# Kernel optimization log

Measured on AMD Instinct MI355X. Metric: run time of the kernel, lower is better.

The kernel has to match this reference:

```python
import jax, jax.numpy as jnp
import numpy as np

B, N, F, T, O, E = 4, 30000, 32, 12, 64, 480000


def setup_inputs() -> dict:
    key = jax.random.key(0)
    ks = jax.random.split(key, 20)
    s = 0.05
    inp = {
        "X": jax.random.normal(ks[0], (B, N, F, T), dtype=jnp.float32),
        "edge_index": jax.random.randint(ks[1], (2, E), 0, N, dtype=jnp.int64),
        # GCNConv weights for the three gates (num_layers=1 -> single conv each)
        "Wg_z": jax.random.normal(ks[2], (F, O), dtype=jnp.float32) * s,
        "bg_z": jnp.zeros((O,), jnp.float32),
        "Wg_r": jax.random.normal(ks[3], (F, O), dtype=jnp.float32) * s,
        "bg_r": jnp.zeros((O,), jnp.float32),
        "Wg_h": jax.random.normal(ks[4], (F, O), dtype=jnp.float32) * s,
        "bg_h": jnp.zeros((O,), jnp.float32),
        # gate Linear(2*O, O) weights
        "Wl_z": jax.random.normal(ks[5], (2 * O, O), dtype=jnp.float32) * s,
        "bl_z": jnp.zeros((O,), jnp.float32),
        "Wl_r": jax.random.normal(ks[6], (2 * O, O), dtype=jnp.float32) * s,
        "bl_r": jnp.zeros((O,), jnp.float32),
        "Wl_h": jax.random.normal(ks[7], (2 * O, O), dtype=jnp.float32) * s,
        "bl_h": jnp.zeros((O,), jnp.float32),
        # A3TGCN per-period attention and final readout Linear(O, T)
        "att": jax.random.normal(ks[8], (T,), dtype=jnp.float32),
        "W_out": jax.random.normal(ks[9], (O, T), dtype=jnp.float32) * s,
        "b_out": jnp.zeros((T,), jnp.float32),
    }
    return inp


def reference(X, edge_index, Wg_z, bg_z, Wg_r, bg_r, Wg_h, bg_h,
              Wl_z, bl_z, Wl_r, bl_r, Wl_h, bl_h, att, W_out, b_out):
    src, dst = edge_index[0], edge_index[1]
    n = X.shape[1]
    # GCN symmetric normalization with self-loops: deg = in-degree + 1
    deg = jnp.zeros((n,), X.dtype).at[dst].add(1.0) + 1.0
    dis = jax.lax.rsqrt(deg)  # deg^{-1/2}
    edge_norm = (dis[src] * dis[dst])[None, :, None]  # [1,E,1]
    self_norm = (dis * dis)[None, :, None]            # [1,N,1]

    def gcn_conv(x, W, b):  # x: [B,N,F] -> [B,N,O]
        xw = jnp.einsum('bnf,fo->bno', x, W)
        agg = jnp.zeros_like(xw).at[:, dst, :].add(xw[:, src, :] * edge_norm)
        return agg + xw * self_norm + b

    H0 = jnp.zeros((X.shape[0], n, Wg_z.shape[1]), X.dtype)  # H defaults to zeros
    probs = jax.nn.softmax(att)

    def step(acc, inp):
        x_t, p = inp  # x_t: [B,N,F]
        Z = jax.nn.sigmoid(jnp.concatenate([gcn_conv(x_t, Wg_z, bg_z), H0], -1) @ Wl_z + bl_z)
        R = jax.nn.sigmoid(jnp.concatenate([gcn_conv(x_t, Wg_r, bg_r), H0], -1) @ Wl_r + bl_r)
        Ht = jnp.tanh(jnp.concatenate([gcn_conv(x_t, Wg_h, bg_h), H0 * R], -1) @ Wl_h + bl_h)
        Hn = Z * H0 + (1.0 - Z) * Ht
        return acc + p * Hn, None

    Xt = jnp.moveaxis(X, -1, 0)  # [T,B,N,F]
    H_acc, _ = jax.lax.scan(step, jnp.zeros_like(H0), (Xt, probs))
    # TemporalGNN head: ReLU + Linear(O, periods)
    return jax.nn.relu(H_acc) @ W_out + b_out  # [B,N,T]
```

## Files before the change

kernel.cpp:

```cpp
#include <hip/hip_runtime.h>
#include <hip/hip_bf16.h>
#include <hip/hip_fp16.h>


#define FDIM 32
#define TDIM 12
#define ODIM 64
#define BDIM 4

typedef _Float16 half8v __attribute__((ext_vector_type(8)));
typedef float float4v __attribute__((ext_vector_type(4)));

__global__ __launch_bounds__(256) void kA(
    const float4* __restrict__ Xin, uint2* __restrict__ Xh, int n4, int cvtB,
    const int* __restrict__ dstE, int* __restrict__ counts, int E, int cntB,
    const float* __restrict__ Wg_z, const float* __restrict__ bg_z,
    const float* __restrict__ Wl_z, const float* __restrict__ bl_z,
    const float* __restrict__ Wg_h, const float* __restrict__ bg_h,
    const float* __restrict__ Wl_h, const float* __restrict__ bl_h,
    const float* __restrict__ att,
    float* __restrict__ Wz, float* __restrict__ bz,
    float* __restrict__ Wh, float* __restrict__ bh,
    float* __restrict__ probs) {
    const int bid = blockIdx.x;
    const int tid = threadIdx.x;
    if (bid < cvtB) {
        int i = bid * 256 + tid;
        const int stride = cvtB * 256;
        for (; i < n4; i += stride) {
            const float4 v = Xin[i];
            __half2 h0 = __floats2half2_rn(v.x, v.y);
            __half2 h1 = __floats2half2_rn(v.z, v.w);
            uint2 u;
            u.x = *reinterpret_cast<unsigned*>(&h0);
            u.y = *reinterpret_cast<unsigned*>(&h1);
            Xh[i] = u;
        }
    } else if (bid < cvtB + cntB) {
        int e = (bid - cvtB) * 256 + tid;
        if (e < E) atomicAdd(&counts[dstE[e]], 1);
    } else {
        for (int i = tid; i < FDIM * ODIM; i += 256) {
            int f = i >> 6, o = i & 63;
            float az = 0.f, ah = 0.f;
            for (int k = 0; k < ODIM; k++) {
                az += Wg_z[f * ODIM + k] * Wl_z[k * ODIM + o];
                ah += Wg_h[f * ODIM + k] * Wl_h[k * ODIM + o];
            }
            Wz[i] = az;
            Wh[i] = ah;
        }
        if (tid < ODIM) {
            float az = bl_z[tid], ah = bl_h[tid];
            for (int k = 0; k < ODIM; k++) {
                az += bg_z[k] * Wl_z[k * ODIM + tid];
                ah += bg_h[k] * Wl_h[k * ODIM + tid];
            }
            bz[tid] = az;
            bh[tid] = ah;
        }
        if (tid == 0) {
            float m = -1e30f;
            for (int t = 0; t < TDIM; t++) m = fmaxf(m, att[t]);
            float e[TDIM], s = 0.f;
            for (int t = 0; t < TDIM; t++) { e[t] = expf(att[t] - m); s += e[t]; }
            for (int t = 0; t < TDIM; t++) probs[t] = e[t] / s;
        }
    }
}

__global__ __launch_bounds__(1024) void k_scan(const int* __restrict__ counts,
                                               int* __restrict__ offsets,
                                               float* __restrict__ dis,
                                               int* __restrict__ fill,
                                               int2* __restrict__ csr, int N) {
    __shared__ int wsum[16];
    __shared__ int sCarry;
    const int tid = threadIdx.x;
    const int lane = tid & 63;
    const int wv = tid >> 6;
    if (tid == 0) sCarry = 0;
    __syncthreads();
    for (int base = 0; base < N; base += 1024) {
        int i = base + tid;
        int v = (i < N) ? (counts[i] + 1) : 0;
        int s = v;
        for (int off = 1; off < 64; off <<= 1) {
            int t = __shfl_up(s, off, 64);
            if (lane >= off) s += t;
        }
        if (lane == 63) wsum[wv] = s;
        __syncthreads();
        if (wv == 0 && lane < 16) {
            int ws = wsum[lane];
            for (int off = 1; off < 16; off <<= 1) {
                int t = __shfl_up(ws, off, 64);
                if (lane >= off) ws += t;
            }
            wsum[lane] = ws;
        }
        __syncthreads();
        int carry = sCarry;
        int wpre = (wv > 0) ? wsum[wv - 1] : 0;
        if (i < N) {
            const int off0 = carry + wpre + s - v;
            offsets[i] = off0;
            const float d = 1.0f / sqrtf((float)v);
            dis[i] = d;
            fill[i] = 1;
            const float nm = d * d;
            __half2 mh = __floats2half2_rn(nm, nm);
            csr[off0] = make_int2(i, *(int*)&mh);
        }
        __syncthreads();
        if (tid == 0) sCarry = carry + wsum[15];
        __syncthreads();
    }
    if (tid == 0) offsets[N] = sCarry;
}

__global__ void k_scatter(const int* __restrict__ src, const int* __restrict__ dst,
                          const int* __restrict__ offsets, int* __restrict__ fill,
                          const float* __restrict__ dis,
                          int2* __restrict__ csr, int E) {
    int e = blockIdx.x * 256 + threadIdx.x;
    if (e < E) {
        int s = src[e], d = dst[e];
        int pos = offsets[d] + atomicAdd(&fill[d], 1);
        float nm = dis[s] * dis[d];
        __half2 mh = __floats2half2_rn(nm, nm);
        csr[pos] = make_int2(s, *(int*)&mh);
    }
}

__device__ __forceinline__ float sigm(float x) { return 1.f / (1.f + __expf(-x)); }
__device__ __forceinline__ float tanhfast(float x) { return 1.f - 2.f / (1.f + __expf(2.f * x)); }

#define HPACC(mhI, v, hs0, hs1, hs2, hs3)                                      \
    {                                                                          \
        int mi_ = (mhI);                                                       \
        __half2 mh_ = *(__half2*)&mi_;                                         \
        hs0 = __hfma2(mh_, *(__half2*)&(v).x, hs0);                            \
        hs1 = __hfma2(mh_, *(__half2*)&(v).y, hs1);                            \
        hs2 = __hfma2(mh_, *(__half2*)&(v).z, hs2);                            \
        hs3 = __hfma2(mh_, *(__half2*)&(v).w, hs3);                            \
    }

#define HFLUSH(hs0, hs1, hs2, hs3)                                             \
    {                                                                          \
        float2 t_;                                                             \
        t_ = __half22float2(hs0); a0 += t_.x; a1 += t_.y;                      \
        t_ = __half22float2(hs1); a2 += t_.x; a3 += t_.y;                      \
        t_ = __half22float2(hs2); a4 += t_.x; a5 += t_.y;                      \
        t_ = __half22float2(hs3); a6 += t_.x; a7 += t_.y;                      \
        hs0 = hzero; hs1 = hzero; hs2 = hzero; hs3 = hzero;                    \
    }

#define LOADB(dst, Wsrc, jt)                                                   \
    {                                                                          \
        _Pragma("unroll") for (int r_ = 0; r_ < 8; r_++)                       \
            dst[r_] = (_Float16)Wsrc[(kg * 8 + r_) * ODIM + (jt) * 16 + c];    \
    }

#define EPI(qv, dzv, dhv, bzv, bhv)                                            \
    {                                                                          \
        float s_ = 0.f;                                                        \
        {  const float zf_ = dzv[0] + bzv, hf_ = dhv[0] + bhv;                 \
           const float u_ = __expf(-zf_), v_ = __expf(2.f * hf_);              \
           s_ += pr0 * u_ * (v_ - 1.f) *                                       \
                 __builtin_amdgcn_rcpf((1.f + u_) * (1.f + v_)); }             \
        {  const float zf_ = dzv[1] + bzv, hf_ = dhv[1] + bhv;                 \
           const float u_ = __expf(-zf_), v_ = __expf(2.f * hf_);              \
           s_ += pr1 * u_ * (v_ - 1.f) *                                       \
                 __builtin_amdgcn_rcpf((1.f + u_) * (1.f + v_)); }             \
        {  const float zf_ = dzv[2] + bzv, hf_ = dhv[2] + bhv;                 \
           const float u_ = __expf(-zf_), v_ = __expf(2.f * hf_);              \
           s_ += pr2 * u_ * (v_ - 1.f) *                                       \
                 __builtin_amdgcn_rcpf((1.f + u_) * (1.f + v_)); }             \
        {  const float zf_ = dzv[3] + bzv, hf_ = dhv[3] + bhv;                 \
           const float u_ = __expf(-zf_), v_ = __expf(2.f * hf_);              \
           s_ += pr3 * u_ * (v_ - 1.f) *                                       \
                 __builtin_amdgcn_rcpf((1.f + u_) * (1.f + v_)); }             \
        s_ += __shfl_xor(s_, 16, 64);                                          \
        s_ += __shfl_xor(s_, 32, 64);                                          \
        qv = s_;                                                               \
    }

__global__ __launch_bounds__(256, 4) void k_main_w(
    const uint4* __restrict__ Xh, const int* __restrict__ offs,
    const int2* __restrict__ csr,
    const float* __restrict__ Wz, const float* __restrict__ bz,
    const float* __restrict__ Wh, const float* __restrict__ bh,
    const float* __restrict__ probs, const float* __restrict__ Wout,
    const float* __restrict__ bout, float* __restrict__ out, int N) {
    __shared__ float sY[4][16 * 36 + 4];

    const int tid = threadIdx.x;
    const int wv = tid >> 6;
    const int lane = tid & 63;
    const int lanec = lane < 47 ? lane : 47;
    const int c = lane & 15;
    const int kg = lane >> 4;

    half8v wzf0, wzf1, wzf2, wzf3, whf0, whf1, whf2, whf3;
    LOADB(wzf0, Wz, 0) LOADB(wzf1, Wz, 1) LOADB(wzf2, Wz, 2) LOADB(wzf3, Wz, 3)
    LOADB(whf0, Wh, 0) LOADB(whf1, Wh, 1) LOADB(whf2, Wh, 2) LOADB(whf3, Wh, 3)
    half8v wo0, wo1;
#pragma unroll
    for (int r_ = 0; r_ < 8; r_++) {
        wo0[r_] = (_Float16)((c < TDIM) ? Wout[(kg * 8 + r_) * TDIM + c] : 0.f);
        wo1[r_] = (_Float16)((c < TDIM) ? Wout[(32 + kg * 8 + r_) * TDIM + c] : 0.f);
    }
    const float bz0 = bz[c], bz1 = bz[16 + c], bz2 = bz[32 + c], bz3 = bz[48 + c];
    const float bh0 = bh[c], bh1 = bh[16 + c], bh2 = bh[32 + c], bh3 = bh[48 + c];
    const float pr0 = (kg * 4 + 0 < TDIM) ? probs[kg * 4 + 0] : 0.f;
    const float pr1 = (kg * 4 + 1 < TDIM) ? probs[kg * 4 + 1] : 0.f;
    const float pr2 = (kg * 4 + 2 < TDIM) ? probs[kg * 4 + 2] : 0.f;
    const float pr3 = (kg * 4 + 3 < TDIM) ? probs[kg * 4 + 3] : 0.f;
    const float bo = (lane < TDIM) ? bout[lane] : 0.f;
    const __half2 hzero = __float2half2_rn(0.f);

    float* __restrict__ sy = sY[wv];
    const int strideT = gridDim.x * 4;
    const int totalTasks = N * BDIM;

    int task0 = blockIdx.x * 4 + wv;
    if (task0 >= totalTasks) return;
    int b = task0 / N;
    int n = task0 - b * N;

    while (true) {
        const int bs = __builtin_amdgcn_readfirstlane(b);
        const int ns = __builtin_amdgcn_readfirstlane(n);
        const unsigned rowB = (unsigned)bs * (unsigned)N;
        const int begS = __builtin_amdgcn_readfirstlane(offs[ns]);
        const int endS = __builtin_amdgcn_readfirstlane(offs[ns + 1]);

        float a0 = 0.f, a1 = 0.f, a2 = 0.f, a3 = 0.f,
              a4 = 0.f, a5 = 0.f, a6 = 0.f, a7 = 0.f;
        __half2 hA0 = hzero, hA1 = hzero, hA2 = hzero, hA3 = hzero;
        __half2 hB0 = hzero, hB1 = hzero, hB2 = hzero, hB3 = hzero;
        int j = begS;
        for (; j + 8 <= endS; j += 8) {
            const int2 e0 = csr[j + 0], e1 = csr[j + 1], e2 = csr[j + 2], e3 = csr[j + 3];
            const int2 e4 = csr[j + 4], e5 = csr[j + 5], e6 = csr[j + 6], e7 = csr[j + 7];
            const uint4 x0 = Xh[(rowB + (unsigned)e0.x) * 48u + lanec];
            const uint4 x1 = Xh[(rowB + (unsigned)e1.x) * 48u + lanec];
            const uint4 x2 = Xh[(rowB + (unsigned)e2.x) * 48u + lanec];
            const uint4 x3 = Xh[(rowB + (unsigned)e3.x) * 48u + lanec];
            const uint4 x4 = Xh[(rowB + (unsigned)e4.x) * 48u + lanec];
            const uint4 x5 = Xh[(rowB + (unsigned)e5.x) * 48u + lanec];
            const uint4 x6 = Xh[(rowB + (unsigned)e6.x) * 48u + lanec];
            const uint4 x7 = Xh[(rowB + (unsigned)e7.x) * 48u + lanec];
            HPACC(e0.y, x0, hA0, hA1, hA2, hA3);
            HPACC(e1.y, x1, hA0, hA1, hA2, hA3);
            HPACC(e2.y, x2, hA0, hA1, hA2, hA3);
            HPACC(e3.y, x3, hA0, hA1, hA2, hA3);
            HPACC(e4.y, x4, hB0, hB1, hB2, hB3);
            HPACC(e5.y, x5, hB0, hB1, hB2, hB3);
            HPACC(e6.y, x6, hB0, hB1, hB2, hB3);
            HPACC(e7.y, x7, hB0, hB1, hB2, hB3);
            HFLUSH(hA0, hA1, hA2, hA3);
            HFLUSH(hB0, hB1, hB2, hB3);
        }
        for (; j < endS; ++j) {
            const int2 e = csr[j];
            const uint4 xv = Xh[(rowB + (unsigned)e.x) * 48u + lanec];
            HPACC(e.y, xv, hA0, hA1, hA2, hA3);
        }
        HFLUSH(hA0, hA1, hA2, hA3);

        if (lane < 48) {
            int flat = lane * 8;
            int f = flat / 12;
            int t = flat - f * 12;
#pragma unroll
            for (int k = 0; k < 8; k++) {
                float av = (k == 0) ? a0 : (k == 1) ? a1 : (k == 2) ? a2 :
                           (k == 3) ? a3 : (k == 4) ? a4 : (k == 5) ? a5 :
                           (k == 6) ? a6 : a7;
                sy[t * 36 + f] = av;
                t++;
                if (t == TDIM) { t = 0; f++; }
            }
        }

        half8v af;
        if (c < TDIM) {
            const float4* yp = (const float4*)&sy[c * 36 + kg * 8];
            const float4 y0 = yp[0];
            const float4 y1 = yp[1];
            af[0] = (_Float16)y0.x; af[1] = (_Float16)y0.y;
            af[2] = (_Float16)y0.z; af[3] = (_Float16)y0.w;
            af[4] = (_Float16)y1.x; af[5] = (_Float16)y1.y;
            af[6] = (_Float16)y1.z; af[7] = (_Float16)y1.w;
        } else {
            af[0] = (_Float16)0.f; af[1] = (_Float16)0.f;
            af[2] = (_Float16)0.f; af[3] = (_Float16)0.f;
            af[4] = (_Float16)0.f; af[5] = (_Float16)0.f;
            af[6] = (_Float16)0.f; af[7] = (_Float16)0.f;
        }

        const float4v zero4 = {0.f, 0.f, 0.f, 0.f};
        float4v dz0 = __builtin_amdgcn_mfma_f32_16x16x32_f16(af, wzf0, zero4, 0, 0, 0);
        float4v dz1 = __builtin_amdgcn_mfma_f32_16x16x32_f16(af, wzf1, zero4, 0, 0, 0);
        float4v dz2 = __builtin_amdgcn_mfma_f32_16x16x32_f16(af, wzf2, zero4, 0, 0, 0);
        float4v dz3 = __builtin_amdgcn_mfma_f32_16x16x32_f16(af, wzf3, zero4, 0, 0, 0);
        float4v dh0 = __builtin_amdgcn_mfma_f32_16x16x32_f16(af, whf0, zero4, 0, 0, 0);
        float4v dh1 = __builtin_amdgcn_mfma_f32_16x16x32_f16(af, whf1, zero4, 0, 0, 0);
        float4v dh2 = __builtin_amdgcn_mfma_f32_16x16x32_f16(af, whf2, zero4, 0, 0, 0);
        float4v dh3 = __builtin_amdgcn_mfma_f32_16x16x32_f16(af, whf3, zero4, 0, 0, 0);

        float q0, q1, q2, q3;
        EPI(q0, dz0, dh0, bz0, bh0)
        EPI(q1, dz1, dh1, bz1, bh1)
        EPI(q2, dz2, dh2, bz2, bh2)
        EPI(q3, dz3, dh3, bz3, bh3)
        const float accOwn = (kg == 0) ? q0 : (kg == 1) ? q1 : (kg == 2) ? q2 : q3;

        const float r = fmaxf(accOwn, 0.f);
        half8v ra0, ra1;
#pragma unroll
        for (int j2 = 0; j2 < 8; j2++) {
            ra0[j2] = (_Float16)__shfl(r, (kg << 3) + j2, 64);
            ra1[j2] = (_Float16)__shfl(r, 32 + (kg << 3) + j2, 64);
        }
        float4v dro = __builtin_amdgcn_mfma_f32_16x16x32_f16(ra0, wo0, zero4, 0, 0, 0);
        dro = __builtin_amdgcn_mfma_f32_16x16x32_f16(ra1, wo1, dro, 0, 0, 0);
        if (lane < TDIM)
            out[(rowB + (unsigned)n) * TDIM + lane] = dro[0] + bo;

        n += strideT;
        if (n >= N) { n -= N; b++; }
        if (b >= BDIM) break;
    }
}

__global__ __launch_bounds__(384) void k_main_f(
    const float* __restrict__ X, const int* __restrict__ offsets,
    const int2* __restrict__ csr, const float* __restrict__ dis,
    const float* __restrict__ Wz, const float* __restrict__ bz,
    const float* __restrict__ Wh, const float* __restrict__ bh,
    const float* __restrict__ probs, const float* __restrict__ Wout,
    const float* __restrict__ bout, float* __restrict__ out, int N) {
    const int tid = threadIdx.x;
    const int lane = tid & 63;

    __shared__ float4 sY4[BDIM][96];
    __shared__ float sAcc[BDIM][ODIM];
    __shared__ float sWout[ODIM * TDIM];
    __shared__ float sBout[TDIM];

    for (int i = tid; i < ODIM * TDIM; i += 384) sWout[i] = Wout[i];
    if (tid < TDIM) sBout[tid] = bout[tid];

    const int o = tid & 63;
    const int w = tid >> 6;
    float wzr[FDIM], whr[FDIM];
#pragma unroll
    for (int f = 0; f < FDIM; f++) {
        wzr[f] = Wz[f * ODIM + o];
        whr[f] = Wh[f * ODIM + o];
    }
    const float bzo = bz[o], bho = bh[o];
    const int t0 = w, t1 = w + 6;
    const float p0 = probs[t0], p1 = probs[t1];

    const int b = tid / 96;
    const int q = tid - b * 96;
    const float4* __restrict__ Xq = (const float4*)X;
    const unsigned rowBase = (unsigned)b * (unsigned)N;

    for (int n = blockIdx.x; n < N; n += gridDim.x) {
        if (tid < BDIM * ODIM) ((float*)sAcc)[tid] = 0.f;

        const int beg = offsets[n], end = offsets[n + 1];
        float4 A0 = make_float4(0.f, 0.f, 0.f, 0.f);
        float4 A1 = A0, A2 = A0, A3 = A0;

        for (int ebase = beg; ebase < end; ebase += 64) {
            const int cnt2 = min(64, end - ebase);
            int esrc = 0;
            float enm = 0.f;
            if (ebase + lane < end) {
                const int2 e = csr[ebase + lane];
                esrc = e.x;
                int ey = e.y;
                enm = __half22float2(*(__half2*)&ey).x;
            }
            int j = 0;
            for (; j + 4 <= cnt2; j += 4) {
                const int s0 = __shfl(esrc, j + 0, 64), s1 = __shfl(esrc, j + 1, 64);
                const int s2 = __shfl(esrc, j + 2, 64), s3 = __shfl(esrc, j + 3, 64);
                const float m0 = __shfl(enm, j + 0, 64), m1 = __shfl(enm, j + 1, 64);
                const float m2 = __shfl(enm, j + 2, 64), m3 = __shfl(enm, j + 3, 64);
                const float4 u0 = Xq[(rowBase + s0) * 96u + q];
                const float4 u1 = Xq[(rowBase + s1) * 96u + q];
                const float4 u2 = Xq[(rowBase + s2) * 96u + q];
                const float4 u3 = Xq[(rowBase + s3) * 96u + q];
                A0.x += m0 * u0.x; A0.y += m0 * u0.y; A0.z += m0 * u0.z; A0.w += m0 * u0.w;
                A1.x += m1 * u1.x; A1.y += m1 * u1.y; A1.z += m1 * u1.z; A1.w += m1 * u1.w;
                A2.x += m2 * u2.x; A2.y += m2 * u2.y; A2.z += m2 * u2.z; A2.w += m2 * u2.w;
                A3.x += m3 * u3.x; A3.y += m3 * u3.y; A3.z += m3 * u3.z; A3.w += m3 * u3.w;
            }
            for (; j < cnt2; j++) {
                const int s = __shfl(esrc, j, 64);
                const float m = __shfl(enm, j, 64);
                const float4 u = Xq[(rowBase + s) * 96u + q];
                A0.x += m * u.x; A0.y += m * u.y; A0.z += m * u.z; A0.w += m * u.w;
            }
        }
        A0.x += (A1.x + A2.x) + A3.x;
        A0.y += (A1.y + A2.y) + A3.y;
        A0.z += (A1.z + A2.z) + A3.z;
        A0.w += (A1.w + A2.w) + A3.w;
        sY4[b][q] = A0;
        __syncthreads();

#pragma unroll
        for (int bb = 0; bb < BDIM; bb++) {
            const float* yb = (const float*)sY4[bb];
            float z0 = bzo, z1 = bzo, h0 = bho, h1 = bho;
#pragma unroll
            for (int f = 0; f < FDIM; f++) {
                float ya = yb[f * TDIM + t0];
                float yc = yb[f * TDIM + t1];
                z0 += ya * wzr[f]; h0 += ya * whr[f];
                z1 += yc * wzr[f]; h1 += yc * whr[f];
            }
            float contrib = p0 * (1.f - sigm(z0)) * tanhfast(h0)
                          + p1 * (1.f - sigm(z1)) * tanhfast(h1);
            atomicAdd(&sAcc[bb][o], contrib);
        }
        __syncthreads();

        if (tid < BDIM * TDIM) {
            int ob = tid / TDIM, jj = tid - ob * TDIM;
            float v = sBout[jj];
#pragma unroll
            for (int o2 = 0; o2 < ODIM; o2++) {
                v += fmaxf(sAcc[ob][o2], 0.f) * sWout[o2 * TDIM + jj];
            }
            out[(unsigned)(ob * N + n) * TDIM + jj] = v;
        }
        __syncthreads();
    }
}

extern "C" void kernel_launch(void* const* d_in, const int* in_sizes, int n_in,
                              void* d_out, int out_size, void* d_ws, size_t ws_size,
                              hipStream_t stream) {
    const float* X    = (const float*)d_in[0];
    const int*   ei   = (const int*)d_in[1];
    const float* Wg_z = (const float*)d_in[2];
    const float* bg_z = (const float*)d_in[3];
    const float* Wg_h = (const float*)d_in[6];
    const float* bg_h = (const float*)d_in[7];
    const float* Wl_z = (const float*)d_in[8];
    const float* bl_z = (const float*)d_in[9];
    const float* Wl_h = (const float*)d_in[12];
    const float* bl_h = (const float*)d_in[13];
    const float* att  = (const float*)d_in[14];
    const float* Wout = (const float*)d_in[15];
    const float* bout = (const float*)d_in[16];
    float* out = (float*)d_out;

    const int E = in_sizes[1] / 2;
    const int N = in_sizes[0] / (BDIM * FDIM * TDIM);
    const size_t xElems = (size_t)BDIM * N * FDIM * TDIM;
    const size_t xhBytes = xElems * 2;
    const size_t csrBytes = (size_t)(E + N) * 8;
    const size_t restBytes = (size_t)N * 4 * 4 + 64 + csrBytes + 20000;
    const bool useH = ws_size >= xhBytes + restBytes;

    char* wp = (char*)d_ws;
    uint2* Xh = nullptr;
    if (useH) { Xh = (uint2*)wp; wp += xhBytes; }
    int* counts   = (int*)wp;   wp += (size_t)N * 4;
    int* fill     = (int*)wp;   wp += (size_t)N * 4;
    int* offs     = (int*)wp;   wp += (size_t)(N + 4) * 4;
    float* dis    = (float*)wp; wp += (size_t)N * 4;
    int2* csr     = (int2*)wp;  wp += csrBytes;
    float* Wz     = (float*)wp; wp += FDIM * ODIM * 4;
    float* Wh     = (float*)wp; wp += FDIM * ODIM * 4;
    float* bz     = (float*)wp; wp += ODIM * 4;
    float* bh     = (float*)wp; wp += ODIM * 4;
    float* probs  = (float*)wp; wp += 16 * 4;

    hipMemsetAsync(counts, 0, (size_t)N * 4, stream);

    const int cvtB = useH ? 2048 : 0;
    const int cntB = (E + 255) / 256;
    const int n4 = (int)(xElems / 4);
    kA<<<cvtB + cntB + 1, 256, 0, stream>>>(
        (const float4*)X, Xh, n4, cvtB,
        ei + E, counts, E, cntB,
        Wg_z, bg_z, Wl_z, bl_z, Wg_h, bg_h, Wl_h, bl_h, att,
        Wz, bz, Wh, bh, probs);
    k_scan<<<1, 1024, 0, stream>>>(counts, offs, dis, fill, csr, N);
    k_scatter<<<(E + 255) / 256, 256, 0, stream>>>(ei, ei + E, offs, fill, dis, csr, E);

    if (useH) {
        k_main_w<<<2048, 256, 0, stream>>>((const uint4*)Xh, offs, csr,
                                           Wz, bz, Wh, bh, probs, Wout, bout, out, N);
    } else {
        int nB = N < 2048 ? N : 2048;
        k_main_f<<<nB, 384, 0, stream>>>(X, offs, csr, dis, Wz, bz, Wh, bh,
                                         probs, Wout, bout, out, N);
    }
}
```

Baseline: 371.6 us.

## Replace single-block degree prefix scan with multi-block reduce-then-scan

The serial one-block scan over all N node degrees is split into two kernels. The first computes per-tile sums across about 30 blocks, and the second has each block add up the earlier partials itself before doing a local scan that writes offsets, dis and the self-loop CSR entries. This is meant to remove the latency of the single 1024-thread block looping about 30 times with barriers. The cost is one extra kernel launch and a small redundant serial sum of partials in each block. The final offset is now written as E+N directly.

```diff
diff --git a/kernel.cpp b/kernel.cpp
--- a/kernel.cpp
+++ b/kernel.cpp
@@ -7,6 +7,7 @@
 #define TDIM 12
 #define ODIM 64
 #define BDIM 4
+#define SCAN_TILE 1024
 
 typedef _Float16 half8v __attribute__((ext_vector_type(8)));
 typedef float float4v __attribute__((ext_vector_type(4)));
@@ -69,54 +70,75 @@
     }
 }
 
-__global__ __launch_bounds__(1024) void k_scan(const int* __restrict__ counts,
-                                               int* __restrict__ offsets,
-                                               float* __restrict__ dis,
-                                               int* __restrict__ fill,
-                                               int2* __restrict__ csr, int N) {
-    __shared__ int wsum[16];
-    __shared__ int sCarry;
+__global__ __launch_bounds__(256) void kB1(const int* __restrict__ counts, int N,
+                                           int* __restrict__ partials) {
+    __shared__ int wsum[4];
     const int tid = threadIdx.x;
+    const int blk = blockIdx.x;
+    const int i0 = blk * SCAN_TILE + tid * 4;
+    int s = 0;
+    s += (i0 + 0 < N) ? counts[i0 + 0] + 1 : 0;
+    s += (i0 + 1 < N) ? counts[i0 + 1] + 1 : 0;
+    s += (i0 + 2 < N) ? counts[i0 + 2] + 1 : 0;
+    s += (i0 + 3 < N) ? counts[i0 + 3] + 1 : 0;
+    for (int off = 1; off < 64; off <<= 1) s += __shfl_xor(s, off, 64);
+    if ((tid & 63) == 0) wsum[tid >> 6] = s;
+    __syncthreads();
+    if (tid == 0) partials[blk] = wsum[0] + wsum[1] + wsum[2] + wsum[3];
+}
+
+__global__ __launch_bounds__(256) void kB3(const int* __restrict__ counts, int N,
+                                           const int* __restrict__ partials,
+                                           int* __restrict__ offsets,
+                                           float* __restrict__ dis,
+                                           int* __restrict__ fill,
+                                           int2* __restrict__ csr, int E) {
+    __shared__ int sBase;
+    __shared__ int wsum[4];
+    const int tid = threadIdx.x;
+    const int blk = blockIdx.x;
     const int lane = tid & 63;
     const int wv = tid >> 6;
-    if (tid == 0) sCarry = 0;
+
+    if (tid == 0) {
+        int acc = 0;
+        for (int j = 0; j < blk; j++) acc += partials[j];
+        sBase = acc;
+    }
+
+    const int i0 = blk * SCAN_TILE + tid * 4;
+    const int e0 = (i0 + 0 < N) ? counts[i0 + 0] + 1 : 0;
+    const int e1 = (i0 + 1 < N) ? counts[i0 + 1] + 1 : 0;
+    const int e2 = (i0 + 2 < N) ? counts[i0 + 2] + 1 : 0;
+    const int e3 = (i0 + 3 < N) ? counts[i0 + 3] + 1 : 0;
+    const int s = e0 + e1 + e2 + e3;
+    int inc = s;
+    for (int off = 1; off < 64; off <<= 1) {
+        int t = __shfl_up(inc, off, 64);
+        if (lane >= off) inc += t;
+    }
+    if (lane == 63) wsum[wv] = inc;
     __syncthreads();
-    for (int base = 0; base < N; base += 1024) {
-        int i = base + tid;
-        int v = (i < N) ? (counts[i] + 1) : 0;
-        int s = v;
-        for (int off = 1; off < 64; off <<= 1) {
-            int t = __shfl_up(s, off, 64);
-            if (lane >= off) s += t;
-        }
-        if (lane == 63) wsum[wv] = s;
-        __syncthreads();
-        if (wv == 0 && lane < 16) {
-            int ws = wsum[lane];
-            for (int off = 1; off < 16; off <<= 1) {
-                int t = __shfl_up(ws, off, 64);
-                if (lane >= off) ws += t;
-            }
-            wsum[lane] = ws;
-        }
-        __syncthreads();
-        int carry = sCarry;
-        int wpre = (wv > 0) ? wsum[wv - 1] : 0;
+    int wbase = 0;
+    for (int j = 0; j < wv; j++) wbase += wsum[j];
+    int base = sBase + wbase + inc - s;
+
+    const int ee[4] = {e0, e1, e2, e3};
+#pragma unroll
+    for (int k = 0; k < 4; k++) {
+        const int i = i0 + k;
         if (i < N) {
-            const int off0 = carry + wpre + s - v;
-            offsets[i] = off0;
-            const float d = 1.0f / sqrtf((float)v);
+            offsets[i] = base;
+            const float d = 1.0f / sqrtf((float)ee[k]);
             dis[i] = d;
             fill[i] = 1;
             const float nm = d * d;
             __half2 mh = __floats2half2_rn(nm, nm);
-            csr[off0] = make_int2(i, *(int*)&mh);
-        }
-        __syncthreads();
-        if (tid == 0) sCarry = carry + wsum[15];
-        __syncthreads();
-    }
-    if (tid == 0) offsets[N] = sCarry;
+            csr[base] = make_int2(i, *(int*)&mh);
+            base += ee[k];
+        }
+    }
+    if (blk == 0 && tid == 0) offsets[N] = E + N;
 }
 
 __global__ void k_scatter(const int* __restrict__ src, const int* __restrict__ dst,
@@ -470,8 +492,9 @@
     const size_t xElems = (size_t)BDIM * N * FDIM * TDIM;
     const size_t xhBytes = xElems * 2;
     const size_t csrBytes = (size_t)(E + N) * 8;
-    const size_t restBytes = (size_t)N * 4 * 4 + 64 + csrBytes + 20000;
+    const size_t restBytes = (size_t)N * 4 * 4 + 4096 + csrBytes + 20000;
     const bool useH = ws_size >= xhBytes + restBytes;
+    const int nScanBlk = (N + SCAN_TILE - 1) / SCAN_TILE;
 
     char* wp = (char*)d_ws;
     uint2* Xh = nullptr;
@@ -480,6 +503,7 @@
     int* fill     = (int*)wp;   wp += (size_t)N * 4;
     int* offs     = (int*)wp;   wp += (size_t)(N + 4) * 4;
     float* dis    = (float*)wp; wp += (size_t)N * 4;
+    int* partials = (int*)wp;   wp += (size_t)(nScanBlk + 4) * 4;
     int2* csr     = (int2*)wp;  wp += csrBytes;
     float* Wz     = (float*)wp; wp += FDIM * ODIM * 4;
     float* Wh     = (float*)wp; wp += FDIM * ODIM * 4;
@@ -497,7 +521,8 @@
         ei + E, counts, E, cntB,
         Wg_z, bg_z, Wl_z, bl_z, Wg_h, bg_h, Wl_h, bl_h, att,
         Wz, bz, Wh, bh, probs);
-    k_scan<<<1, 1024, 0, stream>>>(counts, offs, dis, fill, csr, N);
+    kB1<<<nScanBlk, 256, 0, stream>>>(counts, N, partials);
+    kB3<<<nScanBlk, 256, 0, stream>>>(counts, N, partials, offs, dis, fill, csr, E);
     k_scatter<<<(E + 255) / 256, 256, 0, stream>>>(ei, ei + E, offs, fill, dis, csr, E);
 
     if (useH) {
```

Measured after the change: 335.6 us. -9.7%, faster.
